# Performance work log

Measured on AMD Instinct MI355X. Metric: run time of the kernel, lower is better.

The kernel has to match this reference:

```python
import jax, jax.numpy as jnp
import numpy as np

B = 1048576
IN_DIM = 2
TIME_DIM = 1
HID = 128


def _linear_params(key, fan_in, fan_out):
    kw, kb = jax.random.split(key)
    bound = 1.0 / np.sqrt(fan_in)
    W = jax.random.uniform(kw, (fan_in, fan_out), minval=-bound, maxval=bound, dtype=jnp.float32)
    b = jax.random.uniform(kb, (fan_out,), minval=-bound, maxval=bound, dtype=jnp.float32)
    return W, b


def setup_inputs() -> dict:
    key = jax.random.key(0)
    ks = jax.random.split(key, 7)
    x = jax.random.normal(ks[0], (B, IN_DIM), dtype=jnp.float32)
    t = jax.random.uniform(ks[1], (B,), dtype=jnp.float32)
    W1, b1 = _linear_params(ks[2], IN_DIM + TIME_DIM, HID)
    W2, b2 = _linear_params(ks[3], HID, HID)
    W3, b3 = _linear_params(ks[4], HID, HID)
    W4, b4 = _linear_params(ks[5], HID, HID)
    W5, b5 = _linear_params(ks[6], HID, IN_DIM)
    return {"x": x, "t": t,
            "W1": W1, "b1": b1, "W2": W2, "b2": b2,
            "W3": W3, "b3": b3, "W4": W4, "b4": b4,
            "W5": W5, "b5": b5}


def _swish(h):
    return h * jax.nn.sigmoid(h)


def reference(x, t, W1, b1, W2, b2, W3, b3, W4, b4, W5, b5):
    sz = x.shape
    xf = x.reshape(-1, IN_DIM)
    tf = t.reshape(-1, TIME_DIM).astype(jnp.float32)
    tf = jnp.broadcast_to(tf.reshape(-1, 1), (xf.shape[0], 1))
    h = jnp.concatenate([xf, tf], axis=1)  # (B, 3)
    h = _swish(h @ W1 + b1)
    h = _swish(h @ W2 + b2)
    h = _swish(h @ W3 + b3)
    h = _swish(h @ W4 + b4)
    out = h @ W5 + b5  # (B, 2)
    return out.reshape(sz)
```

## Files before the change

kernel.cpp:

```cpp
#include <hip/hip_runtime.h>

typedef _Float16 half8  __attribute__((ext_vector_type(8)));
typedef __fp16   fp16x2 __attribute__((ext_vector_type(2)));
typedef float    f32x16 __attribute__((ext_vector_type(16)));
typedef float    f32x4v __attribute__((ext_vector_type(4)));
typedef unsigned uint2v __attribute__((ext_vector_type(2)));

#define NWG     256
#define WGSZ    512
#define CHUNKS  8
#define WFRAG0   0
#define WFRAG1   8192
#define WFRAG2   16384
#define W1FRAGO  24576
#define W5FRAGO  25600
#define BIASO    27648
#define B5O      28160
#define SMEM_U32 28164

#define FENCE() __builtin_amdgcn_sched_barrier(0)

__device__ __forceinline__ unsigned pack_rn(float a, float b) {
  unsigned lo = (unsigned)__builtin_bit_cast(unsigned short, (_Float16)a);
  unsigned hi = (unsigned)__builtin_bit_cast(unsigned short, (_Float16)b);
  return lo | (hi << 16);
}
__device__ __forceinline__ unsigned pack_rtz(float a, float b) {
  fp16x2 h = __builtin_amdgcn_cvt_pkrtz(a, b);
  return __builtin_bit_cast(unsigned, h);
}
__device__ __forceinline__ float sw(float v) {
  float e = __builtin_amdgcn_exp2f(v * -1.44269504089f);
  return v * __builtin_amdgcn_rcpf(1.0f + e);
}
__device__ __forceinline__ half8 ldfrag(const unsigned* p) {
  uint4 u = *reinterpret_cast<const uint4*>(p);
  return __builtin_bit_cast(half8, u);
}
__device__ __forceinline__ half8 mkfrag(unsigned a, unsigned b, unsigned c, unsigned d) {
  uint4 u = make_uint4(a, b, c, d);
  return __builtin_bit_cast(half8, u);
}

__device__ __forceinline__ void pl_swap(unsigned &a, unsigned &b) {
#if __has_builtin(__builtin_amdgcn_permlane32_swap)
  uint2v r = __builtin_amdgcn_permlane32_swap(a, b, false, false);
  a = r.x; b = r.y;
#else
  asm("v_permlane32_swap_b32 %0, %1" : "+v"(a), "+v"(b));
#endif
}

__device__ __forceinline__ void build_b(const unsigned (&p)[8], half8 &bf0, half8 &bf1) {
  unsigned a0 = p[0], a2 = p[2];
  unsigned a1 = p[1], a3 = p[3];
  unsigned a4 = p[4], a6 = p[6];
  unsigned a5 = p[5], a7 = p[7];
  pl_swap(a0, a2);
  pl_swap(a1, a3);
  pl_swap(a4, a6);
  pl_swap(a5, a7);
  bf0 = mkfrag(a0, a1, a2, a3);
  bf1 = mkfrag(a4, a5, a6, a7);
}

__device__ __forceinline__ void layer32(const unsigned (&pin)[4][8], unsigned (&pout)[4][8],
                                        const unsigned* wb, const float* bias, int h5, int lane) {
#pragma unroll
  for (int mi = 0; mi < 4; ++mi) {
    f32x16 acc;
#pragma unroll
    for (int g = 0; g < 4; ++g) {
      f32x4v bv = *reinterpret_cast<const f32x4v*>(bias + 32*mi + 8*g + 4*h5);
#pragma unroll
      for (int q = 0; q < 4; ++q) acc[4*g+q] = bv[q];
    }
#pragma unroll
    for (int ks = 0; ks < 4; ++ks) {
      half8 bf0, bf1;
      build_b(pin[ks], bf0, bf1);
      half8 a0 = ldfrag(wb + (((2*ks  )*4 + mi)*64 + lane)*4);
      acc = __builtin_amdgcn_mfma_f32_32x32x16_f16(a0, bf0, acc, 0, 0, 0);
      half8 a1 = ldfrag(wb + (((2*ks+1)*4 + mi)*64 + lane)*4);
      acc = __builtin_amdgcn_mfma_f32_32x32x16_f16(a1, bf1, acc, 0, 0, 0);
    }
#pragma unroll
    for (int p = 0; p < 8; ++p)
      pout[mi][p] = pack_rtz(sw(acc[2*p]), sw(acc[2*p+1]));
    FENCE();
  }
}

extern "C" __global__ __launch_bounds__(WGSZ, 1)
void mlp_k(const float* __restrict__ x, const float* __restrict__ t,
           const float* __restrict__ W1, const float* __restrict__ b1,
           const float* __restrict__ W2, const float* __restrict__ b2,
           const float* __restrict__ W3, const float* __restrict__ b3,
           const float* __restrict__ W4, const float* __restrict__ b4,
           const float* __restrict__ W5, const float* __restrict__ b5p,
           float* __restrict__ out)
{
  __shared__ unsigned smem[SMEM_U32];
  const int tid = threadIdx.x;

  {
    const float* Wm[3] = {W2, W3, W4};
#pragma unroll
    for (int L = 0; L < 3; ++L) {
      const float* W = Wm[L];
#pragma unroll 1
      for (int it = 0; it < 16; ++it) {
        int i = it*WGSZ + tid;
        int lane = i & 63, j2 = (i >> 6) & 3, mi = (i >> 8) & 3, kk = i >> 10;
        int k = 16*kk + 8*(lane >> 5) + 2*j2;
        int c = 32*mi + (lane & 31);
        smem[L*8192 + ((kk*4 + mi)*64 + lane)*4 + j2] = pack_rn(W[k*128 + c], W[(k+1)*128 + c]);
      }
    }
  }
#pragma unroll 1
  for (int it = 0; it < 2; ++it) {
    int i = it*WGSZ + tid;
    int lane = i & 63, j2 = (i >> 6) & 3, mi = (i >> 8) & 3;
    int k = 8*(lane >> 5) + 2*j2;
    int c = 32*mi + (lane & 31);
    float a = (k   < 3) ? W1[k*128 + c]     : 0.f;
    float b = (k+1 < 3) ? W1[(k+1)*128 + c] : 0.f;
    smem[W1FRAGO + (mi*64 + lane)*4 + j2] = pack_rn(a, b);
  }
#pragma unroll 1
  for (int it = 0; it < 4; ++it) {
    int i = it*WGSZ + tid;
    int lane = i & 63, j2 = (i >> 6) & 3, kk = (i >> 8) & 7;
    int m = lane & 31;
    int k = 16*kk + 8*(lane >> 5) + 2*j2;
    float a = (m < 2) ? W5[k*2 + m]     : 0.f;
    float b = (m < 2) ? W5[(k+1)*2 + m] : 0.f;
    smem[W5FRAGO + (kk*64 + lane)*4 + j2] = pack_rn(a, b);
  }
  {
    const float* bp = (tid < 128) ? b1 : (tid < 256) ? b2 : (tid < 384) ? b3 : b4;
    smem[BIASO + tid] = __builtin_bit_cast(unsigned, bp[tid & 127]);
    if (tid < 2) smem[B5O + tid] = __builtin_bit_cast(unsigned, b5p[tid]);
  }
  __syncthreads();

  const int lane = tid & 63;
  const int wv   = tid >> 6;
  const int h5   = lane >> 5;
  const int col  = lane & 31;
  const bool lo  = lane < 32;
  const float* biasp = reinterpret_cast<const float*>(smem + BIASO);
  const float b50 = reinterpret_cast<const float*>(smem + B5O)[0];
  const float b51 = reinterpret_cast<const float*>(smem + B5O)[1];
  const float2* x2 = reinterpret_cast<const float2*>(x);

#pragma unroll 1
  for (int ps = 0; ps < CHUNKS*2; ++ps) {
    const int base = ((int)blockIdx.x * CHUNKS + (ps >> 1)) * WGSZ + wv * 64 + 32*(ps & 1);
    const int s = base + col;

    float2 xa = x2[s];
    float  ta = t[s];

    half8 b1f = mkfrag(h5 ? 0u : pack_rn(xa.x, xa.y), h5 ? 0u : pack_rn(ta, 0.f), 0u, 0u);

    unsigned pkA[4][8], pkB[4][8];

#pragma unroll
    for (int mi = 0; mi < 4; ++mi) {
      f32x16 acc;
#pragma unroll
      for (int g = 0; g < 4; ++g) {
        f32x4v bv = *reinterpret_cast<const f32x4v*>(biasp + 32*mi + 8*g + 4*h5);
#pragma unroll
        for (int q = 0; q < 4; ++q) acc[4*g+q] = bv[q];
      }
      half8 a = ldfrag(smem + W1FRAGO + (mi*64 + lane)*4);
      acc = __builtin_amdgcn_mfma_f32_32x32x16_f16(a, b1f, acc, 0, 0, 0);
#pragma unroll
      for (int p = 0; p < 8; ++p)
        pkA[mi][p] = pack_rtz(sw(acc[2*p]), sw(acc[2*p+1]));
      FENCE();
    }

    layer32(pkA, pkB, smem + WFRAG0, biasp + 128, h5, lane);
    layer32(pkB, pkA, smem + WFRAG1, biasp + 256, h5, lane);
    layer32(pkA, pkB, smem + WFRAG2, biasp + 384, h5, lane);

    f32x16 a5;
#pragma unroll
    for (int e = 0; e < 16; ++e) a5[e] = 0.f;
    a5[0] = b50; a5[1] = b51;
#pragma unroll
    for (int ks = 0; ks < 4; ++ks) {
      half8 bf0, bf1;
      build_b(pkB[ks], bf0, bf1);
      half8 a0 = ldfrag(smem + W5FRAGO + ((2*ks  )*64 + lane)*4);
      a5 = __builtin_amdgcn_mfma_f32_32x32x16_f16(a0, bf0, a5, 0, 0, 0);
      half8 a1 = ldfrag(smem + W5FRAGO + ((2*ks+1)*64 + lane)*4);
      a5 = __builtin_amdgcn_mfma_f32_32x32x16_f16(a1, bf1, a5, 0, 0, 0);
    }
    if (lo) {
      reinterpret_cast<float2*>(out)[s] = make_float2(a5[0], a5[1]);
    }
    FENCE();
  }
}

extern "C" void kernel_launch(void* const* d_in, const int* in_sizes, int n_in,
                              void* d_out, int out_size, void* d_ws, size_t ws_size,
                              hipStream_t stream) {
  (void)in_sizes; (void)n_in; (void)d_ws; (void)ws_size; (void)out_size;
  const float* x  = (const float*)d_in[0];
  const float* t  = (const float*)d_in[1];
  const float* W1 = (const float*)d_in[2];
  const float* b1 = (const float*)d_in[3];
  const float* W2 = (const float*)d_in[4];
  const float* b2 = (const float*)d_in[5];
  const float* W3 = (const float*)d_in[6];
  const float* b3 = (const float*)d_in[7];
  const float* W4 = (const float*)d_in[8];
  const float* b4 = (const float*)d_in[9];
  const float* W5 = (const float*)d_in[10];
  const float* b5 = (const float*)d_in[11];
  float* out = (float*)d_out;

  mlp_k<<<dim3(NWG), dim3(WGSZ), 0, stream>>>(x, t, W1, b1, W2, b2, W3, b3, W4, b4, W5, b5, out);
}
```

Before: 258.5 us.

## Fold biases into MFMA via augmented weight slab and restructure layer loop order

```diff
diff --git a/kernel.cpp b/kernel.cpp
--- a/kernel.cpp
+++ b/kernel.cpp
@@ -3,20 +3,18 @@
 typedef _Float16 half8  __attribute__((ext_vector_type(8)));
 typedef __fp16   fp16x2 __attribute__((ext_vector_type(2)));
 typedef float    f32x16 __attribute__((ext_vector_type(16)));
-typedef float    f32x4v __attribute__((ext_vector_type(4)));
 typedef unsigned uint2v __attribute__((ext_vector_type(2)));
 
 #define NWG     256
 #define WGSZ    512
 #define CHUNKS  8
 #define WFRAG0   0
-#define WFRAG1   8192
-#define WFRAG2   16384
-#define W1FRAGO  24576
-#define W5FRAGO  25600
-#define BIASO    27648
-#define B5O      28160
-#define SMEM_U32 28164
+#define WFRAG1   9216
+#define WFRAG2   18432
+#define W1FRAGO  27648
+#define W5FRAGO  28672
+#define B5O      30720
+#define SMEM_U32 30722
 
 #define FENCE() __builtin_amdgcn_sched_barrier(0)
 
@@ -64,31 +62,41 @@
   bf1 = mkfrag(a4, a5, a6, a7);
 }
 
-__device__ __forceinline__ void layer32(const unsigned (&pin)[4][8], unsigned (&pout)[4][8],
-                                        const unsigned* wb, const float* bias, int h5, int lane) {
-#pragma unroll
-  for (int mi = 0; mi < 4; ++mi) {
-    f32x16 acc;
-#pragma unroll
-    for (int g = 0; g < 4; ++g) {
-      f32x4v bv = *reinterpret_cast<const f32x4v*>(bias + 32*mi + 8*g + 4*h5);
-#pragma unroll
-      for (int q = 0; q < 4; ++q) acc[4*g+q] = bv[q];
-    }
-#pragma unroll
-    for (int ks = 0; ks < 4; ++ks) {
-      half8 bf0, bf1;
-      build_b(pin[ks], bf0, bf1);
-      half8 a0 = ldfrag(wb + (((2*ks  )*4 + mi)*64 + lane)*4);
-      acc = __builtin_amdgcn_mfma_f32_32x32x16_f16(a0, bf0, acc, 0, 0, 0);
-      half8 a1 = ldfrag(wb + (((2*ks+1)*4 + mi)*64 + lane)*4);
-      acc = __builtin_amdgcn_mfma_f32_32x32x16_f16(a1, bf1, acc, 0, 0, 0);
-    }
+__device__ __forceinline__ void layer_v2(const unsigned (&pin)[4][8], unsigned (&pout)[4][8],
+                                         const unsigned* wb, unsigned bias_w0, int lane) {
+  half8 bf[4][2];
+#pragma unroll
+  for (int ks = 0; ks < 4; ++ks) build_b(pin[ks], bf[ks][0], bf[ks][1]);
+  FENCE();
+  f32x16 acc[4];
+#pragma unroll
+  for (int mi = 0; mi < 4; ++mi)
+#pragma unroll
+    for (int e = 0; e < 16; ++e) acc[mi][e] = 0.f;
+#pragma unroll
+  for (int kk = 0; kk < 8; ++kk) {
+#pragma unroll
+    for (int mi = 0; mi < 4; ++mi) {
+      half8 a = ldfrag(wb + ((kk*4 + mi)*64 + lane)*4);
+      acc[mi] = __builtin_amdgcn_mfma_f32_32x32x16_f16(a, bf[kk>>1][kk&1], acc[mi], 0, 0, 0);
+    }
+    FENCE();
+  }
+  {
+    half8 bb = mkfrag(bias_w0, 0u, 0u, 0u);
+#pragma unroll
+    for (int mi = 0; mi < 4; ++mi) {
+      half8 a = ldfrag(wb + ((8*4 + mi)*64 + lane)*4);
+      acc[mi] = __builtin_amdgcn_mfma_f32_32x32x16_f16(a, bb, acc[mi], 0, 0, 0);
+    }
+  }
+  FENCE();
+#pragma unroll
+  for (int mi = 0; mi < 4; ++mi)
 #pragma unroll
     for (int p = 0; p < 8; ++p)
-      pout[mi][p] = pack_rtz(sw(acc[2*p]), sw(acc[2*p+1]));
-    FENCE();
-  }
+      pout[mi][p] = pack_rtz(sw(acc[mi][2*p]), sw(acc[mi][2*p+1]));
+  FENCE();
 }
 
 extern "C" __global__ __launch_bounds__(WGSZ, 1)
@@ -105,16 +113,24 @@
 
   {
     const float* Wm[3] = {W2, W3, W4};
+    const float* Bm[3] = {b2, b3, b4};
 #pragma unroll
     for (int L = 0; L < 3; ++L) {
       const float* W = Wm[L];
-#pragma unroll 1
-      for (int it = 0; it < 16; ++it) {
+      const float* Bv = Bm[L];
+#pragma unroll 1
+      for (int it = 0; it < 18; ++it) {
         int i = it*WGSZ + tid;
         int lane = i & 63, j2 = (i >> 6) & 3, mi = (i >> 8) & 3, kk = i >> 10;
-        int k = 16*kk + 8*(lane >> 5) + 2*j2;
         int c = 32*mi + (lane & 31);
-        smem[L*8192 + ((kk*4 + mi)*64 + lane)*4 + j2] = pack_rn(W[k*128 + c], W[(k+1)*128 + c]);
+        unsigned v;
+        if (kk < 8) {
+          int k = 16*kk + 8*(lane >> 5) + 2*j2;
+          v = pack_rn(W[k*128 + c], W[(k+1)*128 + c]);
+        } else {
+          v = (lane < 32 && j2 == 0) ? pack_rn(Bv[c], 0.f) : 0u;
+        }
+        smem[L*9216 + ((kk*4 + mi)*64 + lane)*4 + j2] = v;
       }
     }
   }
@@ -124,8 +140,8 @@
     int lane = i & 63, j2 = (i >> 6) & 3, mi = (i >> 8) & 3;
     int k = 8*(lane >> 5) + 2*j2;
     int c = 32*mi + (lane & 31);
-    float a = (k   < 3) ? W1[k*128 + c]     : 0.f;
-    float b = (k+1 < 3) ? W1[(k+1)*128 + c] : 0.f;
+    float a = (k < 3) ? W1[k*128 + c] : 0.f;
+    float b = (k+1 < 3) ? W1[(k+1)*128 + c] : ((k+1 == 3) ? b1[c] : 0.f);
     smem[W1FRAGO + (mi*64 + lane)*4 + j2] = pack_rn(a, b);
   }
 #pragma unroll 1
@@ -138,11 +154,7 @@
     float b = (m < 2) ? W5[(k+1)*2 + m] : 0.f;
     smem[W5FRAGO + (kk*64 + lane)*4 + j2] = pack_rn(a, b);
   }
-  {
-    const float* bp = (tid < 128) ? b1 : (tid < 256) ? b2 : (tid < 384) ? b3 : b4;
-    smem[BIASO + tid] = __builtin_bit_cast(unsigned, bp[tid & 127]);
-    if (tid < 2) smem[B5O + tid] = __builtin_bit_cast(unsigned, b5p[tid]);
-  }
+  if (tid < 2) smem[B5O + tid] = __builtin_bit_cast(unsigned, b5p[tid]);
   __syncthreads();
 
   const int lane = tid & 63;
@@ -150,7 +162,7 @@
   const int h5   = lane >> 5;
   const int col  = lane & 31;
   const bool lo  = lane < 32;
-  const float* biasp = reinterpret_cast<const float*>(smem + BIASO);
+  const unsigned bias_w0 = h5 ? 0u : 0x00003C00u;
   const float b50 = reinterpret_cast<const float*>(smem + B5O)[0];
   const float b51 = reinterpret_cast<const float*>(smem + B5O)[1];
   const float2* x2 = reinterpret_cast<const float2*>(x);
@@ -163,7 +175,8 @@
     float2 xa = x2[s];
     float  ta = t[s];
 
-    half8 b1f = mkfrag(h5 ? 0u : pack_rn(xa.x, xa.y), h5 ? 0u : pack_rn(ta, 0.f), 0u, 0u);
+    half8 b1f = mkfrag(h5 ? 0u : pack_rn(xa.x, xa.y),
+                       h5 ? 0u : pack_rn(ta, 1.0f), 0u, 0u);
 
     unsigned pkA[4][8], pkB[4][8];
 
@@ -171,11 +184,7 @@
     for (int mi = 0; mi < 4; ++mi) {
       f32x16 acc;
 #pragma unroll
-      for (int g = 0; g < 4; ++g) {
-        f32x4v bv = *reinterpret_cast<const f32x4v*>(biasp + 32*mi + 8*g + 4*h5);
-#pragma unroll
-        for (int q = 0; q < 4; ++q) acc[4*g+q] = bv[q];
-      }
+      for (int e = 0; e < 16; ++e) acc[e] = 0.f;
       half8 a = ldfrag(smem + W1FRAGO + (mi*64 + lane)*4);
       acc = __builtin_amdgcn_mfma_f32_32x32x16_f16(a, b1f, acc, 0, 0, 0);
 #pragma unroll
@@ -184,9 +193,9 @@
       FENCE();
     }
 
-    layer32(pkA, pkB, smem + WFRAG0, biasp + 128, h5, lane);
-    layer32(pkB, pkA, smem + WFRAG1, biasp + 256, h5, lane);
-    layer32(pkA, pkB, smem + WFRAG2, biasp + 384, h5, lane);
+    layer_v2(pkA, pkB, smem + WFRAG0, bias_w0, lane);
+    layer_v2(pkB, pkA, smem + WFRAG1, bias_w0, lane);
+    layer_v2(pkA, pkB, smem + WFRAG2, bias_w0, lane);
 
     f32x16 a5;
 #pragma unroll
```

New measurement: 260.8 us. No clear change (+0.9%).
